# Kernel tuning notes

Hardware: AMD Instinct MI355X
Metric: run time of the kernel (lower is better)

Reference implementation:

```python
import jax, jax.numpy as jnp
import numpy as np
from jax import lax

DIM = 1152
HEADS = 16
HEAD_DIM = 72  # HEADS*HEAD_DIM == DIM
HID = 4608     # int(DIM*4.0)
B = 2
N = 4096
EPS_RMS = 1e-6
EPS_LA = 1e-15


def setup_inputs() -> dict:
    key = jax.random.key(0)
    ks = jax.random.split(key, 12)
    w = lambda k, shape: (jax.random.normal(k, shape, jnp.float32) * 0.02)
    z = lambda n: jnp.zeros((n,), jnp.float32)
    return {
        "hidden_states": jax.random.normal(ks[0], (B, N, DIM), jnp.float32),
        "temb": jax.random.normal(ks[1], (B, 6 * DIM), jnp.float32),
        "scale_shift_table": jax.random.normal(ks[2], (6, DIM), jnp.float32) / np.float32(np.sqrt(DIM)),
        "Wq": w(ks[3], (DIM, DIM)), "bq": z(DIM),
        "Wk": w(ks[4], (DIM, DIM)), "bk": z(DIM),
        "Wv": w(ks[5], (DIM, DIM)), "bv": z(DIM),
        "Wo": w(ks[6], (DIM, DIM)), "bo": z(DIM),
        "W_inv": w(ks[7], (2 * HID, DIM)), "b_inv": z(2 * HID),   # 1x1 conv dim -> 2*hid
        "W_dw": w(ks[8], (2 * HID, 3)), "b_dw": z(2 * HID),       # depthwise k=3
        "W_pt": w(ks[9], (DIM, HID)),                              # 1x1 conv hid -> dim, no bias
    }


def _rms(x):
    # RMSNorm, elementwise_affine=False, eps=1e-6
    return x * lax.rsqrt(jnp.mean(x * x, axis=-1, keepdims=True) + EPS_RMS)


def reference(hidden_states, temb, scale_shift_table, Wq, bq, Wk, bk, Wv, bv, Wo, bo,
              W_inv, b_inv, W_dw, b_dw, W_pt):
    Bn, Nn, D = hidden_states.shape
    # adaLN-single modulation
    mods = scale_shift_table[None] + temb.reshape(Bn, 6, D)  # (B,6,D)
    shift_msa, scale_msa, gate_msa, shift_mlp, scale_mlp, gate_mlp = (
        mods[:, i][:, None, :] for i in range(6))  # each (B,1,D)

    x = _rms(hidden_states) * (1.0 + scale_msa) + shift_msa

    # --- Lite linear attention (ReLU kernel, denominator via padded-ones value) ---
    q = jax.nn.relu(x @ Wq.T + bq).reshape(Bn, Nn, HEADS, HEAD_DIM).transpose(0, 2, 1, 3)  # bhnd
    k = jax.nn.relu(x @ Wk.T + bk).reshape(Bn, Nn, HEADS, HEAD_DIM).transpose(0, 2, 1, 3)
    v = (x @ Wv.T + bv).reshape(Bn, Nn, HEADS, HEAD_DIM).transpose(0, 2, 1, 3)
    v = jnp.pad(v, ((0, 0), (0, 0), (0, 0), (0, 1)), constant_values=1.0)  # (B,h,N,d+1)
    kv = jnp.einsum('bhnd,bhne->bhde', k, v)        # (B,h,d,d+1)
    out = jnp.einsum('bhnd,bhde->bhne', q, kv)      # (B,h,N,d+1)
    out = out[..., :-1] / (out[..., -1:] + EPS_LA)  # numerator / denominator
    out = out.transpose(0, 2, 1, 3).reshape(Bn, Nn, D)
    attn_out = out @ Wo.T + bo

    hidden_states = gate_msa * attn_out + hidden_states

    # --- GLUMBConv FFN ---
    y = _rms(hidden_states) * (1.0 + scale_mlp) + shift_mlp
    y = jax.nn.silu(y @ W_inv.T + b_inv)            # inverted 1x1 conv + SiLU, (B,N,2*HID)
    yc = y.transpose(0, 2, 1)                        # (B,2*HID,N)
    yc = lax.conv_general_dilated(
        yc, W_dw[:, None, :], window_strides=(1,), padding=[(1, 1)],
        feature_group_count=2 * HID,
        dimension_numbers=('NCH', 'OIH', 'NCH')) + b_dw[None, :, None]
    xg, gate = jnp.split(yc, 2, axis=1)
    y = (xg * jax.nn.silu(gate)).transpose(0, 2, 1)  # (B,N,HID)
    ff = y @ W_pt.T                                   # point conv, no bias

    return hidden_states + gate_mlp * ff
```

## Files before the change

### kernel.cpp

```cpp
#include <hip/hip_runtime.h>
#include <hip/hip_bf16.h>

typedef __hip_bfloat16 bf16;
typedef short short8 __attribute__((ext_vector_type(8)));
typedef short short4v __attribute__((ext_vector_type(4)));
typedef float floatx4 __attribute__((ext_vector_type(4)));
typedef int int4v __attribute__((ext_vector_type(4)));

#define DIMC 1152
#define NTOK 8192
#define NSEQ 4096
#define HD 72
#define HDP 73
#define HIDC 4608
#define HID2 9216
#define QKVN 3456
#define KVH (HD * HDP)
#define PZ ((size_t)2048 * DIMC)
#define PZB ((size_t)4096 * DIMC)

#define DP 96
#define KVNT 128
#define KV_NITER 2
#define KV_CHUNKS 16

__device__ __forceinline__ float b2f(bf16 x) { return __bfloat162float(x); }
__device__ __forceinline__ bf16 f2b(float x) { return __float2bfloat16(x); }
__device__ __forceinline__ void st(float* p, float v) { *p = v; }
__device__ __forceinline__ void st(bf16* p, float v)  { *p = f2b(v); }
__device__ __forceinline__ float tf(float x) { return x; }
__device__ __forceinline__ float tf(bf16 x)  { return __bfloat162float(x); }
__device__ __forceinline__ float s2f(short s) {
    unsigned int u = ((unsigned int)(unsigned short)s) << 16;
    return __uint_as_float(u);
}
__device__ __forceinline__ short f2s(float f) {
    bf16 h = f2b(f);
    return *reinterpret_cast<short*>(&h);
}

__device__ __forceinline__ void gload_lds16(const bf16* g, short* l) {
    __builtin_amdgcn_global_load_lds(
        (const __attribute__((address_space(1))) void*)g,
        (__attribute__((address_space(3))) void*)l, 16, 0, 0);
}

__global__ void cvt_all_kernel(const float* __restrict__ s0, const float* __restrict__ s1,
                               const float* __restrict__ s2, const float* __restrict__ s3,
                               const float* __restrict__ s4, const float* __restrict__ s5,
                               bf16* __restrict__ dstA, bf16* __restrict__ dstB) {
    int i = blockIdx.x * 256 + threadIdx.x;
    if (i >= 5308416) return;
    const float* src; int base, ib; bf16* dst;
    if (i < 1327104) {
        dst = dstA; ib = i;
        if (i < 331776)      { src = s0; base = 0; }
        else if (i < 663552) { src = s1; base = 331776; }
        else if (i < 995328) { src = s2; base = 663552; }
        else                 { src = s3; base = 995328; }
    } else {
        dst = dstB; ib = i - 1327104;
        if (i < 3981312)     { src = s4; base = 1327104; }
        else                 { src = s5; base = 3981312; }
    }
    floatx4 v = ((const floatx4*)src)[i - base];
    bf16* o = dst + (size_t)ib * 4;
    o[0] = f2b(v[0]); o[1] = f2b(v[1]); o[2] = f2b(v[2]); o[3] = f2b(v[3]);
}

__global__ void prep_kernel(const float* __restrict__ sst, const float* __restrict__ temb,
                            float* __restrict__ mods, const float* __restrict__ ba,
                            const float* __restrict__ bb, const float* __restrict__ bc,
                            float* __restrict__ bq) {
    int i = blockIdx.x * 256 + threadIdx.x;
    if (i < 2 * 6 * DIMC) {
        mods[i] = sst[i % (6 * DIMC)] + temb[i];
    } else if (i < 2 * 6 * DIMC + DIMC) {
        int j = i - 2 * 6 * DIMC;
        bq[j] = ba[j]; bq[j + DIMC] = bb[j]; bq[j + 2 * DIMC] = bc[j];
    }
}

template<typename T>
__global__ void rmsmod_kernel(const T* __restrict__ h, const float* __restrict__ mods,
                              int shift_idx, int scale_idx, bf16* __restrict__ xout) {
    int token = blockIdx.x;
    int b = token >> 12;
    int tid = threadIdx.x;
    int wave = tid >> 6, lane = tid & 63;
    const T* hp = h + (size_t)token * DIMC;

    float v[8];
    float s = 0.f;
    if (tid < 144) {
        if constexpr (sizeof(T) == 4) {
            floatx4 a = *(const floatx4*)((const float*)hp + tid * 8);
            floatx4 c = *(const floatx4*)((const float*)hp + tid * 8 + 4);
            v[0]=a[0]; v[1]=a[1]; v[2]=a[2]; v[3]=a[3];
            v[4]=c[0]; v[5]=c[1]; v[6]=c[2]; v[7]=c[3];
        } else {
            short8 a = *(const short8*)((const short*)hp + tid * 8);
            #pragma unroll
            for (int j = 0; j < 8; j++) v[j] = s2f(a[j]);
        }
        #pragma unroll
        for (int j = 0; j < 8; j++) s += v[j] * v[j];
    }
    #pragma unroll
    for (int off = 32; off > 0; off >>= 1) s += __shfl_down(s, off);
    __shared__ float wsum[4];
    if (lane == 0) wsum[wave] = s;
    __syncthreads();
    float tot = wsum[0] + wsum[1] + wsum[2] + wsum[3];
    float r = rsqrtf(tot / (float)DIMC + 1e-6f);

    if (tid < 144) {
        const float* sh = mods + (size_t)(b * 6 + shift_idx) * DIMC + tid * 8;
        const float* sc = mods + (size_t)(b * 6 + scale_idx) * DIMC + tid * 8;
        floatx4 sh0 = *(const floatx4*)sh, sh1 = *(const floatx4*)(sh + 4);
        floatx4 sc0 = *(const floatx4*)sc, sc1 = *(const floatx4*)(sc + 4);
        short8 o;
        o[0] = f2s(v[0] * r * (1.f + sc0[0]) + sh0[0]);
        o[1] = f2s(v[1] * r * (1.f + sc0[1]) + sh0[1]);
        o[2] = f2s(v[2] * r * (1.f + sc0[2]) + sh0[2]);
        o[3] = f2s(v[3] * r * (1.f + sc0[3]) + sh0[3]);
        o[4] = f2s(v[4] * r * (1.f + sc1[0]) + sh1[0]);
        o[5] = f2s(v[5] * r * (1.f + sc1[1]) + sh1[1]);
        o[6] = f2s(v[6] * r * (1.f + sc1[2]) + sh1[2]);
        o[7] = f2s(v[7] * r * (1.f + sc1[3]) + sh1[3]);
        *(short8*)((short*)xout + (size_t)token * DIMC + tid * 8) = o;
    }
}

template<int MODE, typename OT>
__global__ __launch_bounds__(256, 2)
void gemm_kernel(const bf16* __restrict__ A, const bf16* __restrict__ W,
                 const float* __restrict__ bias, const float* __restrict__ mods,
                 int gate_idx, int m_off, const float* __restrict__ resid,
                 OT* __restrict__ out, int N, int Kfull, int Klen,
                 size_t zstride, int bm_lo, int bm_hi) {
    const int bm = blockIdx.x;
    if (bm < bm_lo || bm >= bm_hi) return;
    const int koff = blockIdx.z * Klen;
    __shared__ __align__(16) short As[128 * 64];
    __shared__ __align__(16) short Bs[128 * 64];
    const int tid = threadIdx.x;
    const int wave = tid >> 6;
    const int lane = tid & 63;
    const int quad = lane >> 4;
    const int l16 = lane & 15;
    const int wm = (wave & 1) * 64;
    const int wn = (wave >> 1) * 64;
    const int bn = blockIdx.y;

    floatx4 acc[4][4];
    #pragma unroll
    for (int i = 0; i < 4; i++)
        #pragma unroll
        for (int j = 0; j < 4; j++)
            #pragma unroll
            for (int r = 0; r < 4; r++) acc[i][j][r] = 0.0f;

    const int lrow8 = lane >> 3;
    const int scol = ((lane & 7) ^ lrow8) * 8;
    const bf16* gA = A + (size_t)(bm * 128 + wave * 8 + lrow8) * Kfull + koff + scol;
    const bf16* gB = W + (size_t)(bn * 128 + wave * 8 + lrow8) * Kfull + koff + scol;
    short* lA = &As[wave * 512];
    short* lB = &Bs[wave * 512];
    const size_t rstep = (size_t)32 * Kfull;

    for (int k0 = 0; k0 < Klen; k0 += 64) {
        __syncthreads();
        #pragma unroll
        for (int j = 0; j < 4; j++) gload_lds16(gA + j * rstep + k0, lA + j * 2048);
        #pragma unroll
        for (int j = 0; j < 4; j++) gload_lds16(gB + j * rstep + k0, lB + j * 2048);
        __syncthreads();
        short8 af[2][4], bfr[2][4];
        #pragma unroll
        for (int i = 0; i < 4; i++) {
            const int ra = wm + i * 16 + l16;
            const int rb = wn + i * 16 + l16;
            #pragma unroll
            for (int kk = 0; kk < 2; kk++) {
                af[kk][i]  = *(const short8*)&As[ra * 64 + (((kk * 4 + quad) ^ (ra & 7)) * 8)];
                bfr[kk][i] = *(const short8*)&Bs[rb * 64 + (((kk * 4 + quad) ^ (rb & 7)) * 8)];
            }
        }
        #pragma unroll
        for (int kk = 0; kk < 2; kk++)
            #pragma unroll
            for (int i = 0; i < 4; i++)
                #pragma unroll
                for (int j = 0; j < 4; j++)
                    acc[i][j] = __builtin_amdgcn_mfma_f32_16x16x32_bf16(af[kk][i], bfr[kk][j], acc[i][j], 0, 0, 0);
    }

    #pragma unroll
    for (int i = 0; i < 4; i++) {
        #pragma unroll
        for (int j = 0; j < 4; j++) {
            const int col = bn * 128 + wn + j * 16 + l16;
            #pragma unroll
            for (int r = 0; r < 4; r++) {
                const int m = bm * 128 + wm + i * 16 + quad * 4 + r;
                float v = acc[i][j][r];
                float o;
                if (MODE == 0) {
                    o = v + bias[col];
                    if (col < 2 * DIMC) o = fmaxf(o, 0.f);
                } else if (MODE == 2) {
                    int b = (m + m_off) >> 12;
                    o = mods[(size_t)(b * 6 + gate_idx) * DIMC + col] * (v + bias[col])
                        + resid[(size_t)m * DIMC + col];
                } else if (MODE == 3) {
                    float sv = v + bias[col];
                    o = sv / (1.f + __expf(-sv));
                } else if (MODE == 6) {
                    const bf16* tr = (const bf16*)resid;
                    int b = m >> 12;
                    o = tf(tr[(size_t)m * DIMC + col])
                        + mods[(size_t)(b * 6 + gate_idx) * DIMC + col] * v;
                } else {
                    o = v;
                }
                st(&out[zstride * blockIdx.z + (size_t)m * N + col], o);
            }
        }
    }
}

template<int NP>
__global__ void reduce_kernel(const float* __restrict__ part, const bf16* __restrict__ trunk,
                              const float* __restrict__ mods, int b, int r0, size_t pstride,
                              float* __restrict__ out) {
    int i4 = (blockIdx.x * 256 + threadIdx.x) * 4;
    int col = i4 % DIMC;
    floatx4 s = *(const floatx4*)(part + i4);
    #pragma unroll
    for (int p = 1; p < NP; ++p) {
        floatx4 t = *(const floatx4*)(part + (size_t)p * pstride + i4);
        s[0] += t[0]; s[1] += t[1]; s[2] += t[2]; s[3] += t[3];
    }
    size_t gidx = ((size_t)b * NSEQ + r0) * DIMC + i4;
    short4v tr = *(const short4v*)((const short*)trunk + gidx);
    floatx4 g = *(const floatx4*)(mods + (size_t)(b * 6 + 5) * DIMC + col);
    floatx4 o;
    #pragma unroll
    for (int j = 0; j < 4; ++j) o[j] = s2f(tr[j]) + g[j] * s[j];
    *(floatx4*)(out + gidx) = o;
}

__device__ __forceinline__ int kvaddr(int row, int n) {
    return row * KVNT + ((((n >> 3) ^ (row & 7))) << 3) + (n & 7);
}

__global__ __launch_bounds__(256, 3)
void attn_kv_kernel(const bf16* __restrict__ qkv, float* __restrict__ part) {
    const int chunk = blockIdx.x;
    const int h = blockIdx.y;
    const int b = blockIdx.z;
    __shared__ __align__(16) short kl[DP * KVNT];
    __shared__ __align__(16) short vl[DP * KVNT];
    const int tid = threadIdx.x;
    const int wave = tid >> 6, lane = tid & 63;
    const int quad = lane >> 4, l16 = lane & 15;
    const int wd = (wave & 1) * 48;
    const int we = (wave >> 1) * 48;

    for (int i = tid; i < 24 * KVNT; i += 256) {
        kl[72 * KVNT + i] = 0;
        vl[72 * KVNT + i] = (i < KVNT) ? (short)0x3F80 : (short)0;
    }

    floatx4 acc[3][3];
    #pragma unroll
    for (int i = 0; i < 3; i++)
        #pragma unroll
        for (int j = 0; j < 3; j++)
            #pragma unroll
            for (int r = 0; r < 4; r++) acc[i][j][r] = 0.0f;

    const size_t tok0 = (size_t)b * NSEQ + (size_t)chunk * (KVNT * KV_NITER);
    for (int it = 0; it < KV_NITER; ++it) {
        __syncthreads();
        const short* rb = (const short*)qkv + (tok0 + (size_t)it * KVNT) * QKVN + h * HD;
        #pragma unroll
        for (int p = 0; p < 5; ++p) {
            int idx = p * 256 + tid;
            int o = idx >> 7, n = idx & 127;
            if (o < 9) {
                const short* g = rb + (size_t)n * QKVN + o * 8;
                short8 kk = *(const short8*)(g + DIMC);
                short8 vv = *(const short8*)(g + 2 * DIMC);
                #pragma unroll
                for (int j = 0; j < 8; ++j) {
                    kl[kvaddr(o * 8 + j, n)] = kk[j];
                    vl[kvaddr(o * 8 + j, n)] = vv[j];
                }
            }
        }
        __syncthreads();
        #pragma unroll
        for (int ks = 0; ks < 4; ++ks) {
            const int nb = ks * 32 + quad * 8;
            short8 af[3], bfv[3];
            #pragma unroll
            for (int i = 0; i < 3; ++i) {
                const int ra = wd + i * 16 + l16;
                const int rbn = we + i * 16 + l16;
                af[i]  = *(const short8*)&kl[ra * KVNT + ((((nb >> 3) ^ (ra & 7))) << 3)];
                bfv[i] = *(const short8*)&vl[rbn * KVNT + ((((nb >> 3) ^ (rbn & 7))) << 3)];
            }
            #pragma unroll
            for (int i = 0; i < 3; ++i)
                #pragma unroll
                for (int j = 0; j < 3; ++j)
                    acc[i][j] = __builtin_amdgcn_mfma_f32_16x16x32_bf16(af[i], bfv[j], acc[i][j], 0, 0, 0);
        }
    }

    float* op = part + ((size_t)((b * 16 + h) * KV_CHUNKS + chunk)) * KVH;
    #pragma unroll
    for (int i = 0; i < 3; ++i) {
        const int dbase = wd + i * 16 + quad * 4;
        #pragma unroll
        for (int j = 0; j < 3; ++j) {
            const int e = we + j * 16 + l16;
            if (e < HDP) {
                #pragma unroll
                for (int r = 0; r < 4; ++r) {
                    const int d = dbase + r;
                    if (d < HD) op[d * HDP + e] = acc[i][j][r];
                }
            }
        }
    }
}

__global__ void kvred_kernel(const float* __restrict__ part, float* __restrict__ kvout) {
    int i = blockIdx.x * 256 + threadIdx.x;
    if (i >= 32 * KVH) return;
    int bh = i / KVH, cell = i - bh * KVH;
    const float* p = part + ((size_t)bh * KV_CHUNKS) * KVH + cell;
    float s = 0.f;
    #pragma unroll
    for (int c = 0; c < KV_CHUNKS; ++c) s += p[(size_t)c * KVH];
    kvout[i] = s;
}

__global__ __launch_bounds__(256, 2)
void attn_out_kernel(const bf16* __restrict__ qkv, const float* __restrict__ kv,
                     bf16* __restrict__ outa) {
    const int chunk = blockIdx.x;
    const int h = blockIdx.y;
    const int b = blockIdx.z;
    __shared__ __align__(16) short ql[128 * 128];
    __shared__ __align__(16) short kvt[80 * 128];
    const int tid = threadIdx.x;
    const int wave = tid >> 6, lane = tid & 63;
    const int quad = lane >> 4, l16 = lane & 15;
    const int wm = wave * 32;

    const short* qbase = (const short*)qkv + ((size_t)(b * NSEQ) + (size_t)chunk * 128) * QKVN + h * HD;
    #pragma unroll
    for (int t = 0; t < 8; ++t) {
        int idx = t * 256 + tid;
        int o = idx >> 7, n = idx & 127;
        short8 vv = {0, 0, 0, 0, 0, 0, 0, 0};
        if (o < 9) vv = *(const short8*)(qbase + (size_t)n * QKVN + o * 8);
        *(short8*)&ql[n * 128 + ((o ^ (n & 7)) << 3)] = vv;
    }
    const float* kp = kv + (size_t)(b * 16 + h) * KVH;
    #pragma unroll
    for (int t = 0; t < 5; ++t) {
        int idx = t * 256 + tid;
        int o = idx / 80, e = idx - (idx / 80) * 80;
        short8 vv = {0, 0, 0, 0, 0, 0, 0, 0};
        if (e < HDP && o < 9) {
            #pragma unroll
            for (int j = 0; j < 8; ++j) {
                int d = o * 8 + j;
                if (d < HD) vv[j] = f2s(kp[(size_t)d * HDP + e]);
            }
        }
        *(short8*)&kvt[e * 128 + ((o ^ (e & 7)) << 3)] = vv;
    }
    __syncthreads();

    floatx4 acc[2][5];
    #pragma unroll
    for (int i = 0; i < 2; ++i)
        #pragma unroll
        for (int j = 0; j < 5; ++j)
            #pragma unroll
            for (int r = 0; r < 4; ++r) acc[i][j][r] = 0.0f;

    #pragma unroll
    for (int kk = 0; kk < 3; ++kk) {
        const int s = kk * 4 + quad;
        short8 af[2];
        #pragma unroll
        for (int i = 0; i < 2; ++i) {
            const int ra = wm + i * 16 + l16;
            af[i] = *(const short8*)&ql[ra * 128 + ((s ^ (ra & 7)) << 3)];
        }
        #pragma unroll
        for (int j = 0; j < 5; ++j) {
            const int rb = j * 16 + l16;
            short8 bfv = *(const short8*)&kvt[rb * 128 + ((s ^ (rb & 7)) << 3)];
            #pragma unroll
            for (int i = 0; i < 2; ++i)
                acc[i][j] = __builtin_amdgcn_mfma_f32_16x16x32_bf16(af[i], bfv, acc[i][j], 0, 0, 0);
        }
    }

    #pragma unroll
    for (int i = 0; i < 2; ++i) {
        #pragma unroll
        for (int r = 0; r < 4; ++r) {
            float den = __shfl(acc[i][4][r], (lane & 48) | 8);
            float inv = 1.0f / (den + 1e-15f);
            const int m = wm + i * 16 + quad * 4 + r;
            bf16* op = outa + ((size_t)(b * NSEQ) + (size_t)chunk * 128 + m) * DIMC + h * HD;
            #pragma unroll
            for (int j = 0; j < 5; ++j) {
                const int e = j * 16 + l16;
                if (e < HD) op[e] = f2b(acc[i][j][r] * inv);
            }
        }
    }
}

__global__ __launch_bounds__(576)
void dwglu_kernel(const bf16* __restrict__ ybuf, const float* __restrict__ wdw,
                  const float* __restrict__ bdw, int r0, int rowoff, bf16* __restrict__ outg) {
    int bid = blockIdx.x;
    int nper = gridDim.x >> 3;
    int nl = (bid & 7) * nper + (bid >> 3);
    int g = (r0 + nl) & (NSEQ - 1);
    int c = threadIdx.x * 8;
    int cg = c + HIDC;
    size_t base = (size_t)(nl + rowoff) * HID2;
    const short* yb = (const short*)ybuf;
    short8 zr = {0, 0, 0, 0, 0, 0, 0, 0};
    bool hm = (g > 0), hp = (g < NSEQ - 1);
    short8 xm = hm ? *(const short8*)(yb + base - HID2 + c)  : zr;
    short8 x0 =      *(const short8*)(yb + base + c);
    short8 xp = hp ? *(const short8*)(yb + base + HID2 + c)  : zr;
    short8 gm = hm ? *(const short8*)(yb + base - HID2 + cg) : zr;
    short8 g0 =      *(const short8*)(yb + base + cg);
    short8 gp = hp ? *(const short8*)(yb + base + HID2 + cg) : zr;
    float wx[24], wg[24], bxv[8], bgv[8];
    #pragma unroll
    for (int t = 0; t < 6; t++) {
        *(floatx4*)&wx[t * 4] = *(const floatx4*)(wdw + (size_t)c * 3 + t * 4);
        *(floatx4*)&wg[t * 4] = *(const floatx4*)(wdw + (size_t)cg * 3 + t * 4);
    }
    *(floatx4*)&bxv[0] = *(const floatx4*)(bdw + c);
    *(floatx4*)&bxv[4] = *(const floatx4*)(bdw + c + 4);
    *(floatx4*)&bgv[0] = *(const floatx4*)(bdw + cg);
    *(floatx4*)&bgv[4] = *(const floatx4*)(bdw + cg + 4);
    short8 o;
    #pragma unroll
    for (int j = 0; j < 8; j++) {
        float a  = s2f(xm[j]) * wx[j * 3] + s2f(x0[j]) * wx[j * 3 + 1]
                 + s2f(xp[j]) * wx[j * 3 + 2] + bxv[j];
        float gg = s2f(gm[j]) * wg[j * 3] + s2f(g0[j]) * wg[j * 3 + 1]
                 + s2f(gp[j]) * wg[j * 3 + 2] + bgv[j];
        float sg = gg / (1.f + __expf(-gg));
        o[j] = f2s(a * sg);
    }
    *(short8*)((short*)outg + (size_t)nl * HIDC + c) = o;
}

extern "C" void kernel_launch(void* const* d_in, const int* in_sizes, int n_in,
                              void* d_out, int out_size, void* d_ws, size_t ws_size,
                              hipStream_t stream) {
    const float* h_in = (const float*)d_in[0];
    const float* temb = (const float*)d_in[1];
    const float* sst  = (const float*)d_in[2];
    const float* Wq = (const float*)d_in[3];   const float* bq_ = (const float*)d_in[4];
    const float* Wk = (const float*)d_in[5];   const float* bk_ = (const float*)d_in[6];
    const float* Wv = (const float*)d_in[7];   const float* bv_ = (const float*)d_in[8];
    const float* Wo = (const float*)d_in[9];   const float* bo_ = (const float*)d_in[10];
    const float* Winv = (const float*)d_in[11]; const float* binv = (const float*)d_in[12];
    const float* Wdw  = (const float*)d_in[13]; const float* bdw  = (const float*)d_in[14];
    const float* Wpt  = (const float*)d_in[15];
    float* out = (float*)d_out;

    const int WSMALL = DIMC * DIMC;
    const int WINVN  = HID2 * DIMC;
    const int WPTN   = DIMC * HIDC;

    char* basep = (char*)d_ws;
    size_t off = 0;
    auto alloc = [&](size_t bytes) -> char* {
        char* p = basep + off;
        off += (bytes + 255) & ~(size_t)255;
        return p;
    };
    float* modsb = (float*)alloc((size_t)2 * 6 * DIMC * 4);
    float* kvb   = (float*)alloc((size_t)32 * KVH * 4);
    float* bqkv  = (float*)alloc((size_t)QKVN * 4);
    bf16* wib  = (bf16*)alloc((size_t)WINVN * 2);
    bf16* wpb  = (bf16*)alloc((size_t)WPTN * 2);
    bf16* trunk = (bf16*)alloc((size_t)NTOK * DIMC * 2);

    const size_t QKVB_B  = (size_t)NTOK * QKVN * 2;
    const size_t BX_B    = (size_t)NTOK * DIMC * 2;
    const size_t BGLU2   = (size_t)NTOK * HIDC * 2;
    const size_t BBIG_B  = (size_t)NSEQ * HID2 * 2;
    const size_t KVPART_B = (size_t)32 * KV_CHUNKS * KVH * 4;
    const size_t WQKV_B  = (size_t)3 * WSMALL * 2;
    const size_t WOB_B   = (size_t)WSMALL * 2;
    const size_t BGLU_B  = (size_t)NSEQ * HIDC * 2;

    bool tier0 = (ws_size >= off + BGLU2 + BBIG_B + 1024);

    bf16 *qkvb, *bx, *wqkv, *wob;
    float* kvpart;
    char* R;
    if (tier0) {
        R = alloc(BGLU2 + BBIG_B);
        qkvb   = (bf16*)R;
        bx     = (bf16*)(R + QKVB_B);
        kvpart = (float*)(R + BGLU2);
        wqkv   = (bf16*)(R + BGLU2 + KVPART_B);
        wob    = (bf16*)(R + BGLU2 + KVPART_B + WQKV_B);
    } else {
        kvpart = (float*)alloc(KVPART_B);
        wqkv   = (bf16*)alloc(WQKV_B);
        wob    = (bf16*)alloc(WOB_B);
        bx     = (bf16*)alloc(BX_B);
        bool tier1 = (ws_size >= off + BGLU_B + BBIG_B + 1024);
        R = alloc(tier1 ? (BGLU_B + BBIG_B) : (size_t)61341696);
        qkvb = (bf16*)R;
        if (!tier1) {  }
    }
    bool tier1 = !tier0 && (ws_size >= ((size_t)(((char*)bx - basep)) + BX_B + 255 + BGLU_B + BBIG_B + 1024));

    cvt_all_kernel<<<20736, 256, 0, stream>>>(Wq, Wk, Wv, Wo, Winv, Wpt, wqkv, wib);
    prep_kernel<<<59, 256, 0, stream>>>(sst, temb, modsb, bq_, bk_, bv_, bqkv);
    rmsmod_kernel<float><<<NTOK, 256, 0, stream>>>(h_in, modsb, 0, 1, bx);

    gemm_kernel<0, bf16><<<dim3(NTOK / 128, QKVN / 128), 256, 0, stream>>>(
        bx, wqkv, bqkv, nullptr, 0, 0, nullptr, qkvb, QKVN, DIMC, DIMC, 0, 0, 1 << 30);

    attn_kv_kernel<<<dim3(KV_CHUNKS, 16, 2), 256, 0, stream>>>(qkvb, kvpart);
    kvred_kernel<<<(32 * KVH + 255) / 256, 256, 0, stream>>>(kvpart, kvb);
    attn_out_kernel<<<dim3(32, 16, 2), 256, 0, stream>>>(qkvb, kvb, bx);
    gemm_kernel<2, bf16><<<dim3(NTOK / 128, DIMC / 128), 256, 0, stream>>>(
        bx, wob, bo_, modsb, 2, 0, h_in, trunk, DIMC, DIMC, DIMC, 0, 0, 1 << 30);
    rmsmod_kernel<bf16><<<NTOK, 256, 0, stream>>>(trunk, modsb, 3, 4, bx);

    if (tier0) {
        bf16* bglu = (bf16*)R;
        bf16* bbig = (bf16*)(R + BGLU2);
        for (int b = 0; b < 2; ++b) {
            const bf16* Ainv = bx + (size_t)b * NSEQ * DIMC;
            gemm_kernel<3, bf16><<<dim3(NSEQ / 128, HID2 / 128), 256, 0, stream>>>(
                Ainv, wib, binv, nullptr, 0, 0, nullptr, bbig, HID2, DIMC, DIMC, 0, 0, 1 << 30);
            dwglu_kernel<<<dim3(NSEQ), 576, 0, stream>>>(
                bbig, Wdw, bdw, 0, 0, bglu + (size_t)b * NSEQ * HIDC);
        }
        gemm_kernel<6, float><<<dim3(NTOK / 128, DIMC / 128), 256, 0, stream>>>(
            bglu, wpb, nullptr, modsb, 5, 0, (const float*)trunk, out, DIMC, HIDC, HIDC,
            0, 0, 1 << 30);
    } else if (tier1) {
        bf16*  bglu = (bf16*)R;
        bf16*  bbig = (bf16*)(R + BGLU_B);
        float* partials = (float*)(R + BGLU_B);
        for (int b = 0; b < 2; ++b) {
            const bf16* Ainv = bx + (size_t)b * NSEQ * DIMC;
            gemm_kernel<3, bf16><<<dim3(NSEQ / 128, HID2 / 128), 256, 0, stream>>>(
                Ainv, wib, binv, nullptr, 0, 0, nullptr, bbig, HID2, DIMC, DIMC, 0, 0, 1 << 30);
            dwglu_kernel<<<dim3(NSEQ), 576, 0, stream>>>(bbig, Wdw, bdw, 0, 0, bglu);
            gemm_kernel<5, float><<<dim3(32, DIMC / 128, 2), 256, 0, stream>>>(
                bglu, wpb, nullptr, nullptr, 0, 0, nullptr, partials, DIMC, HIDC, HIDC / 2,
                PZB, 0, 1 << 30);
            reduce_kernel<2><<<(int)(PZB / 1024), 256, 0, stream>>>(partials, trunk, modsb, b, 0,
                                                                    PZB, out);
        }
    } else {
        bf16*  bglu_c   = (bf16*)R;
        bf16*  bbig_c   = (bf16*)(R + (size_t)18874368);
        float* partials = (float*)(R + (size_t)18874368);
        for (int b = 0; b < 2; ++b) {
            for (int c = 0; c < 2; ++c) {
                int r0 = c * 2048;
                int lo = (c == 0) ? 1 : 0;
                int hi = (c == 0) ? 18 : 17;
                const bf16* Ainv = bx + ((size_t)(b * NSEQ + r0)) * DIMC - (size_t)128 * DIMC;
                gemm_kernel<3, bf16><<<dim3(18, HID2 / 128), 256, 0, stream>>>(
                    Ainv, wib, binv, nullptr, 0, 0, nullptr, bbig_c, HID2, DIMC, DIMC, 0, lo, hi);
                dwglu_kernel<<<dim3(2048), 576, 0, stream>>>(bbig_c, Wdw, bdw, r0, 128, bglu_c);
                gemm_kernel<5, float><<<dim3(16, DIMC / 128, 4), 256, 0, stream>>>(
                    bglu_c, wpb, nullptr, nullptr, 0, 0, nullptr, partials, DIMC, HIDC, HIDC / 4,
                    PZ, 0, 1 << 30);
                reduce_kernel<4><<<(int)(PZ / 1024), 256, 0, stream>>>(partials, trunk, modsb, b,
                                                                       r0, PZ, out);
            }
        }
    }
}
```

Measured before the change: 756.4 us.

## Merge setup kernels, atomically reduce KV, add single-pass FFN tier

Fuses the weight conversion and modulation prep into one setup kernel that also zeroes the KV accumulator. The attention KV kernel now accumulates its chunk partials with atomicAdd straight into the final KV buffer, so the separate reduction kernel and partial buffer go away. When the workspace is large enough, a new tier runs the inverted-conv GEMM and depthwise GLU over both batches in one launch each instead of looping per batch. This cuts the launch count and gives larger grids, at the cost of float atomic contention and a nondeterministic summation order.

```diff
diff --git a/kernel.cpp b/kernel.cpp
--- a/kernel.cpp
+++ b/kernel.cpp
@@ -45,39 +45,43 @@
         (__attribute__((address_space(3))) void*)l, 16, 0, 0);
 }
 
-__global__ void cvt_all_kernel(const float* __restrict__ s0, const float* __restrict__ s1,
-                               const float* __restrict__ s2, const float* __restrict__ s3,
-                               const float* __restrict__ s4, const float* __restrict__ s5,
-                               bf16* __restrict__ dstA, bf16* __restrict__ dstB) {
-    int i = blockIdx.x * 256 + threadIdx.x;
-    if (i >= 5308416) return;
-    const float* src; int base, ib; bf16* dst;
-    if (i < 1327104) {
-        dst = dstA; ib = i;
-        if (i < 331776)      { src = s0; base = 0; }
-        else if (i < 663552) { src = s1; base = 331776; }
-        else if (i < 995328) { src = s2; base = 663552; }
-        else                 { src = s3; base = 995328; }
+__global__ void setup_kernel(const float* __restrict__ s0, const float* __restrict__ s1,
+                             const float* __restrict__ s2, const float* __restrict__ s3,
+                             const float* __restrict__ s4, const float* __restrict__ s5,
+                             bf16* __restrict__ dstA, bf16* __restrict__ dstB,
+                             const float* __restrict__ sst, const float* __restrict__ temb,
+                             float* __restrict__ mods, const float* __restrict__ ba,
+                             const float* __restrict__ bb, const float* __restrict__ bc,
+                             float* __restrict__ bq, float* __restrict__ kvz) {
+    int gb = blockIdx.x;
+    if (gb < 20736) {
+        int i = gb * 256 + threadIdx.x;
+        if (i >= 5308416) return;
+        const float* src; int base, ib; bf16* dst;
+        if (i < 1327104) {
+            dst = dstA; ib = i;
+            if (i < 331776)      { src = s0; base = 0; }
+            else if (i < 663552) { src = s1; base = 331776; }
+            else if (i < 995328) { src = s2; base = 663552; }
+            else                 { src = s3; base = 995328; }
+        } else {
+            dst = dstB; ib = i - 1327104;
+            if (i < 3981312)     { src = s4; base = 1327104; }
+            else                 { src = s5; base = 3981312; }
+        }
+        floatx4 v = ((const floatx4*)src)[i - base];
+        bf16* o = dst + (size_t)ib * 4;
+        o[0] = f2b(v[0]); o[1] = f2b(v[1]); o[2] = f2b(v[2]); o[3] = f2b(v[3]);
     } else {
-        dst = dstB; ib = i - 1327104;
-        if (i < 3981312)     { src = s4; base = 1327104; }
-        else                 { src = s5; base = 3981312; }
-    }
-    floatx4 v = ((const floatx4*)src)[i - base];
-    bf16* o = dst + (size_t)ib * 4;
-    o[0] = f2b(v[0]); o[1] = f2b(v[1]); o[2] = f2b(v[2]); o[3] = f2b(v[3]);
-}
-
-__global__ void prep_kernel(const float* __restrict__ sst, const float* __restrict__ temb,
-                            float* __restrict__ mods, const float* __restrict__ ba,
-                            const float* __restrict__ bb, const float* __restrict__ bc,
-                            float* __restrict__ bq) {
-    int i = blockIdx.x * 256 + threadIdx.x;
-    if (i < 2 * 6 * DIMC) {
-        mods[i] = sst[i % (6 * DIMC)] + temb[i];
-    } else if (i < 2 * 6 * DIMC + DIMC) {
-        int j = i - 2 * 6 * DIMC;
-        bq[j] = ba[j]; bq[j + DIMC] = bb[j]; bq[j + 2 * DIMC] = bc[j];
+        int i = (gb - 20736) * 256 + threadIdx.x;
+        if (i < 13824) {
+            mods[i] = sst[i % (6 * DIMC)] + temb[i];
+        } else if (i < 13824 + DIMC) {
+            int j = i - 13824;
+            bq[j] = ba[j]; bq[j + DIMC] = bb[j]; bq[j + 2 * DIMC] = bc[j];
+        } else if (i < 13824 + DIMC + 32 * KVH) {
+            kvz[i - 13824 - DIMC] = 0.0f;
+        }
     }
 }
 
@@ -256,7 +260,7 @@
 }
 
 __global__ __launch_bounds__(256, 3)
-void attn_kv_kernel(const bf16* __restrict__ qkv, float* __restrict__ part) {
+void attn_kv_kernel(const bf16* __restrict__ qkv, float* __restrict__ kv) {
     const int chunk = blockIdx.x;
     const int h = blockIdx.y;
     const int b = blockIdx.z;
@@ -320,7 +324,7 @@
         }
     }
 
-    float* op = part + ((size_t)((b * 16 + h) * KV_CHUNKS + chunk)) * KVH;
+    float* op = kv + (size_t)(b * 16 + h) * KVH;
     #pragma unroll
     for (int i = 0; i < 3; ++i) {
         const int dbase = wd + i * 16 + quad * 4;
@@ -331,22 +335,11 @@
                 #pragma unroll
                 for (int r = 0; r < 4; ++r) {
                     const int d = dbase + r;
-                    if (d < HD) op[d * HDP + e] = acc[i][j][r];
+                    if (d < HD) atomicAdd(&op[d * HDP + e], acc[i][j][r]);
                 }
             }
         }
     }
-}
-
-__global__ void kvred_kernel(const float* __restrict__ part, float* __restrict__ kvout) {
-    int i = blockIdx.x * 256 + threadIdx.x;
-    if (i >= 32 * KVH) return;
-    int bh = i / KVH, cell = i - bh * KVH;
-    const float* p = part + ((size_t)bh * KV_CHUNKS) * KVH + cell;
-    float s = 0.f;
-    #pragma unroll
-    for (int c = 0; c < KV_CHUNKS; ++c) s += p[(size_t)c * KVH];
-    kvout[i] = s;
 }
 
 __global__ __launch_bounds__(256, 2)
@@ -507,54 +500,58 @@
     bf16* wpb  = (bf16*)alloc((size_t)WPTN * 2);
     bf16* trunk = (bf16*)alloc((size_t)NTOK * DIMC * 2);
 
-    const size_t QKVB_B  = (size_t)NTOK * QKVN * 2;
-    const size_t BX_B    = (size_t)NTOK * DIMC * 2;
-    const size_t BGLU2   = (size_t)NTOK * HIDC * 2;
-    const size_t BBIG_B  = (size_t)NSEQ * HID2 * 2;
-    const size_t KVPART_B = (size_t)32 * KV_CHUNKS * KVH * 4;
-    const size_t WQKV_B  = (size_t)3 * WSMALL * 2;
-    const size_t WOB_B   = (size_t)WSMALL * 2;
-    const size_t BGLU_B  = (size_t)NSEQ * HIDC * 2;
-
-    bool tier0 = (ws_size >= off + BGLU2 + BBIG_B + 1024);
+    const size_t QKVB_B = (size_t)NTOK * QKVN * 2;
+    const size_t BGLU2  = (size_t)NTOK * HIDC * 2;
+    const size_t BBIG_B = (size_t)NSEQ * HID2 * 2;
+    const size_t WQKV_B = (size_t)3 * WSMALL * 2;
+    const size_t WOB_B  = (size_t)WSMALL * 2;
+    const size_t BX_B   = (size_t)NTOK * DIMC * 2;
+    const size_t BGLU_B = (size_t)NSEQ * HIDC * 2;
+
+    bool t0m = (ws_size >= off + BGLU2 + 2 * BBIG_B + 1024);
+    bool t0  = !t0m && (ws_size >= off + BGLU2 + BBIG_B + 1024);
 
     bf16 *qkvb, *bx, *wqkv, *wob;
-    float* kvpart;
     char* R;
-    if (tier0) {
-        R = alloc(BGLU2 + BBIG_B);
-        qkvb   = (bf16*)R;
-        bx     = (bf16*)(R + QKVB_B);
-        kvpart = (float*)(R + BGLU2);
-        wqkv   = (bf16*)(R + BGLU2 + KVPART_B);
-        wob    = (bf16*)(R + BGLU2 + KVPART_B + WQKV_B);
+    bool t1 = false;
+    if (t0m || t0) {
+        R = alloc(BGLU2 + (t0m ? 2 * BBIG_B : BBIG_B));
+        qkvb = (bf16*)R;
+        bx   = (bf16*)(R + QKVB_B);
+        wqkv = (bf16*)(R + BGLU2);
+        wob  = (bf16*)(R + BGLU2 + WQKV_B);
     } else {
-        kvpart = (float*)alloc(KVPART_B);
-        wqkv   = (bf16*)alloc(WQKV_B);
-        wob    = (bf16*)alloc(WOB_B);
-        bx     = (bf16*)alloc(BX_B);
-        bool tier1 = (ws_size >= off + BGLU_B + BBIG_B + 1024);
-        R = alloc(tier1 ? (BGLU_B + BBIG_B) : (size_t)61341696);
+        wqkv = (bf16*)alloc(WQKV_B);
+        wob  = (bf16*)alloc(WOB_B);
+        bx   = (bf16*)alloc(BX_B);
+        t1 = (ws_size >= off + BGLU_B + BBIG_B + 1024);
+        R = alloc(t1 ? (BGLU_B + BBIG_B) : (size_t)61341696);
         qkvb = (bf16*)R;
-        if (!tier1) {  }
-    }
-    bool tier1 = !tier0 && (ws_size >= ((size_t)(((char*)bx - basep)) + BX_B + 255 + BGLU_B + BBIG_B + 1024));
-
-    cvt_all_kernel<<<20736, 256, 0, stream>>>(Wq, Wk, Wv, Wo, Winv, Wpt, wqkv, wib);
-    prep_kernel<<<59, 256, 0, stream>>>(sst, temb, modsb, bq_, bk_, bv_, bqkv);
+    }
+
+    setup_kernel<<<21452, 256, 0, stream>>>(Wq, Wk, Wv, Wo, Winv, Wpt, wqkv, wib,
+                                            sst, temb, modsb, bq_, bk_, bv_, bqkv, kvb);
     rmsmod_kernel<float><<<NTOK, 256, 0, stream>>>(h_in, modsb, 0, 1, bx);
 
     gemm_kernel<0, bf16><<<dim3(NTOK / 128, QKVN / 128), 256, 0, stream>>>(
         bx, wqkv, bqkv, nullptr, 0, 0, nullptr, qkvb, QKVN, DIMC, DIMC, 0, 0, 1 << 30);
 
-    attn_kv_kernel<<<dim3(KV_CHUNKS, 16, 2), 256, 0, stream>>>(qkvb, kvpart);
-    kvred_kernel<<<(32 * KVH + 255) / 256, 256, 0, stream>>>(kvpart, kvb);
+    attn_kv_kernel<<<dim3(KV_CHUNKS, 16, 2), 256, 0, stream>>>(qkvb, kvb);
     attn_out_kernel<<<dim3(32, 16, 2), 256, 0, stream>>>(qkvb, kvb, bx);
     gemm_kernel<2, bf16><<<dim3(NTOK / 128, DIMC / 128), 256, 0, stream>>>(
         bx, wob, bo_, modsb, 2, 0, h_in, trunk, DIMC, DIMC, DIMC, 0, 0, 1 << 30);
     rmsmod_kernel<bf16><<<NTOK, 256, 0, stream>>>(trunk, modsb, 3, 4, bx);
 
-    if (tier0) {
+    if (t0m) {
+        bf16* bglu = (bf16*)R;
+        bf16* bbig = (bf16*)(R + BGLU2);
+        gemm_kernel<3, bf16><<<dim3(NTOK / 128, HID2 / 128), 256, 0, stream>>>(
+            bx, wib, binv, nullptr, 0, 0, nullptr, bbig, HID2, DIMC, DIMC, 0, 0, 1 << 30);
+        dwglu_kernel<<<dim3(NTOK), 576, 0, stream>>>(bbig, Wdw, bdw, 0, 0, bglu);
+        gemm_kernel<6, float><<<dim3(NTOK / 128, DIMC / 128), 256, 0, stream>>>(
+            bglu, wpb, nullptr, modsb, 5, 0, (const float*)trunk, out, DIMC, HIDC, HIDC,
+            0, 0, 1 << 30);
+    } else if (t0) {
         bf16* bglu = (bf16*)R;
         bf16* bbig = (bf16*)(R + BGLU2);
         for (int b = 0; b < 2; ++b) {
@@ -567,7 +564,7 @@
         gemm_kernel<6, float><<<dim3(NTOK / 128, DIMC / 128), 256, 0, stream>>>(
             bglu, wpb, nullptr, modsb, 5, 0, (const float*)trunk, out, DIMC, HIDC, HIDC,
             0, 0, 1 << 30);
-    } else if (tier1) {
+    } else if (t1) {
         bf16*  bglu = (bf16*)R;
         bf16*  bbig = (bf16*)(R + BGLU_B);
         float* partials = (float*)(R + BGLU_B);
```

After: 779.1 us. 1.03x slower.
